# Performance work log

Measured on AMD Instinct MI355X. Metric: run time of the kernel, lower is better.

Reference implementation:

```python
import jax, jax.numpy as jnp
import numpy as np

K = 3          # kernel size
STRIDE = 1
PAD = 1
DIL = 1


def setup_inputs() -> dict:
    key = jax.random.key(0)
    k1, k2, k3 = jax.random.split(key, 3)
    N, Cin, H, W = 8, 128, 64, 64
    Cout = 128
    x = jax.random.normal(k1, (N, Cin, H, W), dtype=jnp.float32)
    # offset channels: 2 * deformable_groups * K*K = 18, interleaved (dy, dx) per tap
    offset = jax.random.normal(k2, (N, 2 * K * K, H, W), dtype=jnp.float32)
    weight = jax.random.normal(k3, (Cout, Cin, K, K), dtype=jnp.float32) / np.sqrt(Cin * K * K)
    return {"x": x, "offset": offset, "weight": weight}


def _deform_conv(x, offset, weight):
    N, Cin, H, W = x.shape
    Cout = weight.shape[0]
    KK = K * K
    Ho, Wo = offset.shape[2], offset.shape[3]

    off = offset.reshape(N, KK, 2, Ho, Wo)
    dy = off[:, :, 0]  # [N, KK, Ho, Wo]
    dx = off[:, :, 1]

    kh = jnp.repeat(jnp.arange(K), K).astype(x.dtype)   # [KK]
    kw = jnp.tile(jnp.arange(K), K).astype(x.dtype)     # [KK]
    base_i = (jnp.arange(Ho) * STRIDE - PAD).astype(x.dtype)  # [Ho]
    base_j = (jnp.arange(Wo) * STRIDE - PAD).astype(x.dtype)  # [Wo]

    # Sampling positions: [N, KK, Ho, Wo]
    py = base_i[None, None, :, None] + (kh * DIL)[None, :, None, None] + dy
    px = base_j[None, None, None, :] + (kw * DIL)[None, :, None, None] + dx

    y0 = jnp.floor(py)
    x0 = jnp.floor(px)
    wy1 = py - y0
    wx1 = px - x0
    wy0 = 1.0 - wy1
    wx0 = 1.0 - wx1
    y0i = y0.astype(jnp.int32)
    x0i = x0.astype(jnp.int32)
    y1i = y0i + 1
    x1i = x0i + 1

    x_flat = x.reshape(N, Cin, H * W)

    def gather(yi, xi):
        # zero-padding outside the image
        mask = ((yi >= 0) & (yi < H) & (xi >= 0) & (xi < W)).astype(x.dtype)
        idx = jnp.clip(yi, 0, H - 1) * W + jnp.clip(xi, 0, W - 1)  # [N,KK,Ho,Wo]
        v = jnp.take_along_axis(x_flat, idx.reshape(N, 1, -1), axis=2)  # [N,Cin,KK*Ho*Wo]
        v = v.reshape(N, Cin, KK, Ho, Wo)
        return v * mask[:, None]

    sampled = (gather(y0i, x0i) * (wy0 * wx0)[:, None]
               + gather(y0i, x1i) * (wy0 * wx1)[:, None]
               + gather(y1i, x0i) * (wy1 * wx0)[:, None]
               + gather(y1i, x1i) * (wy1 * wx1)[:, None])  # [N,Cin,KK,Ho,Wo]

    w = weight.reshape(Cout, Cin, KK)
    return jnp.einsum('nckij,ock->noij', sampled, w)


def reference(x, offset, weight):
    return _deform_conv(x, offset, weight)
```

## Files before the change

kernel.cpp:

```cpp
#include <hip/hip_runtime.h>


#define H  64
#define W  64
#define CIN 128
#define COUT 128
#define NB 8
#define KK 9
#define SROW (CIN + 8)

typedef short bf16x8 __attribute__((ext_vector_type(8)));
typedef float f32x4  __attribute__((ext_vector_type(4)));

__device__ __forceinline__ unsigned short f2bf(float f) {
    unsigned u = __builtin_bit_cast(unsigned, f);
    u += 0x7FFFu + ((u >> 16) & 1u);
    return (unsigned short)(u >> 16);
}
__device__ __forceinline__ unsigned cvt_pk_bf16(float lo, float hi) {
    unsigned r;
    asm("v_cvt_pk_bf16_f32 %0, %1, %2" : "=v"(r) : "v"(lo), "v"(hi));
    return r;
}
__device__ __forceinline__ float lo_f(unsigned u) { return __builtin_bit_cast(float, u << 16); }
__device__ __forceinline__ float hi_f(unsigned u) { return __builtin_bit_cast(float, u & 0xFFFF0000u); }

__global__ void prep_all(const float* __restrict__ x, const float* __restrict__ w,
                         unsigned short* __restrict__ xt, unsigned short* __restrict__ wt) {
    int b = blockIdx.x;
    int t = threadIdx.x;
    if (b >= NB * H) {
        int idx = (b - NB * H) * 256 + t;
        if (idx < KK * COUT * CIN) {
            int e  = idx & 7;
            int lq = (idx >> 3) & 3;
            int lm = (idx >> 5) & 15;
            int ct = (idx >> 9) & 3;
            int nt = (idx >> 11) & 1;
            int c4 = (idx >> 12) & 3;
            int kk = idx >> 14;
            int co = (c4 << 5) + (nt << 4) + lm;
            int ch = (ct << 5) + (lq << 3) + e;
            wt[idx] = f2bf(w[(co * CIN + ch) * KK + kk]);
        }
        return;
    }
    __shared__ float tile[CIN][W + 4];
    int n = b & 7, y = b >> 3;
    const float* src = x + ((size_t)n * CIN * H + y) * W;
    #pragma unroll
    for (int it = 0; it < 8; ++it) {
        int idx = it * 256 + t;
        int c  = idx >> 4;
        int x4 = (idx & 15) << 2;
        int xs = (x4 + ((c >> 5) << 4)) & 63;
        *(float4*)&tile[c][xs] = *(const float4*)(src + (size_t)c * H * W + x4);
    }
    __syncthreads();
    int xp = t >> 2;
    int cbch = (t & 3) << 5;
    int xr = (xp + ((cbch >> 5) << 4)) & 63;
    unsigned short* dst = xt + (((size_t)(n * H + y) * W + xp) * CIN + cbch);
    unsigned rr[16];
    #pragma unroll
    for (int i = 0; i < 16; ++i)
        rr[i] = cvt_pk_bf16(tile[cbch + 2 * i][xr], tile[cbch + 2 * i + 1][xr]);
    #pragma unroll
    for (int i = 0; i < 4; ++i)
        ((uint4*)dst)[i] = make_uint4(rr[4*i], rr[4*i+1], rr[4*i+2], rr[4*i+3]);
}

struct GatherCtx {
    const unsigned short *c00, *c01, *c10, *c11;
    float w00, w01, w10, w11;
};

__device__ __forceinline__ GatherCtx gather_setup(float dy, float dx, int ho, int wo, int kk,
                                                  const unsigned short* xbase) {
    GatherCtx g;
    float py = (float)(ho - 1 + kk / 3) + dy;
    float px = (float)(wo - 1 + kk % 3) + dx;
    float y0f = floorf(py), x0f = floorf(px);
    float wy1 = py - y0f, wx1 = px - x0f;
    float wy0 = 1.f - wy1, wx0 = 1.f - wx1;
    int y0 = (int)y0f, x0 = (int)x0f;
    int y1 = y0 + 1, x1 = x0 + 1;
    bool vy0 = (unsigned)y0 < (unsigned)H, vy1 = (unsigned)y1 < (unsigned)H;
    bool vx0 = (unsigned)x0 < (unsigned)W, vx1 = (unsigned)x1 < (unsigned)W;
    g.w00 = (vy0 && vx0) ? wy0 * wx0 : 0.f;
    g.w01 = (vy0 && vx1) ? wy0 * wx1 : 0.f;
    g.w10 = (vy1 && vx0) ? wy1 * wx0 : 0.f;
    g.w11 = (vy1 && vx1) ? wy1 * wx1 : 0.f;
    int yc0 = min(max(y0, 0), H - 1), yc1 = min(max(y1, 0), H - 1);
    int xc0 = min(max(x0, 0), W - 1), xc1 = min(max(x1, 0), W - 1);
    const unsigned short* r0 = xbase + (size_t)yc0 * W * CIN;
    const unsigned short* r1 = xbase + (size_t)yc1 * W * CIN;
    g.c00 = r0 + xc0 * CIN;  g.c01 = r0 + xc1 * CIN;
    g.c10 = r1 + xc0 * CIN;  g.c11 = r1 + xc1 * CIN;
    return g;
}

__global__ __launch_bounds__(512, 2) void sample_k(
        const float* __restrict__ offs, const unsigned short* __restrict__ xt,
        unsigned short* __restrict__ S) {
    int b = blockIdx.x;
    int n = b & 7;
    int r = b >> 3;
    int tap = r >> 6;
    int ho = r & 63;
    int t = threadIdx.x;
    int pos = t >> 3;
    int cb = (t & 7) << 4;

    const float* offp = offs + ((size_t)(n * 2 * KK + 2 * tap) * H + ho) * W + pos;
    float dy = offp[0];
    float dx = offp[(size_t)H * W];

    GatherCtx g = gather_setup(dy, dx, ho, pos, tap, xt + (size_t)n * H * W * CIN + cb);

    uint4 gv[8];
    #pragma unroll
    for (int j = 0; j < 2; ++j) {
        gv[4*j+0] = *(const uint4*)(g.c00 + 8*j);
        gv[4*j+1] = *(const uint4*)(g.c01 + 8*j);
        gv[4*j+2] = *(const uint4*)(g.c10 + 8*j);
        gv[4*j+3] = *(const uint4*)(g.c11 + 8*j);
    }
    unsigned rr[8];
    #pragma unroll
    for (int j = 0; j < 2; ++j) {
        const unsigned* a0 = (const unsigned*)&gv[4*j+0];
        const unsigned* a1 = (const unsigned*)&gv[4*j+1];
        const unsigned* a2 = (const unsigned*)&gv[4*j+2];
        const unsigned* a3 = (const unsigned*)&gv[4*j+3];
        #pragma unroll
        for (int i = 0; i < 4; ++i) {
            float v0 = g.w00*lo_f(a0[i]) + g.w01*lo_f(a1[i]) + g.w10*lo_f(a2[i]) + g.w11*lo_f(a3[i]);
            float v1 = g.w00*hi_f(a0[i]) + g.w01*hi_f(a1[i]) + g.w10*hi_f(a2[i]) + g.w11*hi_f(a3[i]);
            rr[4*j+i] = cvt_pk_bf16(v0, v1);
        }
    }
    size_t so = ((((size_t)(n * H + ho) * W + pos) * KK + tap) << 7) + cb;
    *(uint4*)(S + so)     = make_uint4(rr[0], rr[1], rr[2], rr[3]);
    *(uint4*)(S + so + 8) = make_uint4(rr[4], rr[5], rr[6], rr[7]);
}

__global__ __launch_bounds__(256, 2) void gemm_k(
        const unsigned short* __restrict__ S, const unsigned short* __restrict__ wt,
        float* __restrict__ out) {
    __shared__ __attribute__((aligned(16))) unsigned short samp[2][64][SROW];

    int b = blockIdx.x;
    int n = b & 7, ho = b >> 3;
    int t = threadIdx.x;
    int lane = t & 63, wv = t >> 6;
    int lm = lane & 15, lq = lane >> 4;
    int cobase = wv << 5;
    int slot = (lm << 2) + lq;

    f32x4 acc[4][2];
    #pragma unroll
    for (int mt = 0; mt < 4; ++mt)
        #pragma unroll
        for (int nt = 0; nt < 2; ++nt) acc[mt][nt] = f32x4{0.f, 0.f, 0.f, 0.f};

    int pos = t >> 2;
    int seg = t & 3;
    const unsigned short* srow = S + ((((size_t)(n * H + ho) * W + pos) * KK) << 7) + (seg << 5);
    const unsigned short* wvbase = wt + ((size_t)wv << 12) + (slot << 3);

    {
        uint4 st[4];
        #pragma unroll
        for (int i = 0; i < 4; ++i) st[i] = *(const uint4*)(srow + (i << 3));
        unsigned short* ld = &samp[0][pos][seg << 5];
        #pragma unroll
        for (int i = 0; i < 4; ++i) *(uint4*)(ld + (i << 3)) = st[i];
    }
    __syncthreads();

    for (int tap = 0; tap < KK; ++tap) {
        uint4 nx[4];
        if (tap < KK - 1) {
            const unsigned short* sr = srow + ((size_t)(tap + 1) << 7);
            #pragma unroll
            for (int i = 0; i < 4; ++i) nx[i] = *(const uint4*)(sr + (i << 3));
        }
        const unsigned short* wkb = wvbase + ((size_t)tap << 14);
        bf16x8 bW[2][4];
        #pragma unroll
        for (int nt = 0; nt < 2; ++nt)
            #pragma unroll
            for (int ct = 0; ct < 4; ++ct)
                bW[nt][ct] = *(const bf16x8*)(wkb + (((nt << 2) + ct) << 9));

        #pragma unroll
        for (int ct = 0; ct < 4; ++ct) {
            bf16x8 a[4];
            #pragma unroll
            for (int mt = 0; mt < 4; ++mt)
                a[mt] = *(const bf16x8*)&samp[tap & 1][lm + (mt << 4)][(ct << 5) + (lq << 3)];
            #pragma unroll
            for (int mt = 0; mt < 4; ++mt) {
                acc[mt][0] = __builtin_amdgcn_mfma_f32_16x16x32_bf16(a[mt], bW[0][ct], acc[mt][0], 0, 0, 0);
                acc[mt][1] = __builtin_amdgcn_mfma_f32_16x16x32_bf16(a[mt], bW[1][ct], acc[mt][1], 0, 0, 0);
            }
        }
        if (tap < KK - 1) {
            unsigned short* ld = &samp[(tap + 1) & 1][pos][seg << 5];
            #pragma unroll
            for (int i = 0; i < 4; ++i) *(uint4*)(ld + (i << 3)) = nx[i];
        }
        __syncthreads();
    }

    #pragma unroll
    for (int mt = 0; mt < 4; ++mt) {
        int wob = (mt << 4) + (lq << 2);
        #pragma unroll
        for (int nt = 0; nt < 2; ++nt) {
            int co = cobase + (nt << 4) + lm;
            *(f32x4*)(out + (((size_t)(n * COUT + co) * H + ho) * W + wob)) = acc[mt][nt];
        }
    }
}

extern "C" void kernel_launch(void* const* d_in, const int* in_sizes, int n_in,
                              void* d_out, int out_size, void* d_ws, size_t ws_size,
                              hipStream_t stream) {
    const float* x      = (const float*)d_in[0];
    const float* offset = (const float*)d_in[1];
    const float* weight = (const float*)d_in[2];
    float* out = (float*)d_out;

    unsigned short* xt = (unsigned short*)d_ws;
    unsigned short* wt = (unsigned short*)((char*)d_ws + 8388608);
    unsigned short* S  = (unsigned short*)((char*)d_ws + 8683520);

    int wblocks = (KK * COUT * CIN + 255) / 256;
    hipLaunchKernelGGL(prep_all, dim3(NB * H + wblocks), dim3(256), 0, stream,
                       x, weight, xt, wt);
    hipLaunchKernelGGL(sample_k, dim3(NB * KK * H), dim3(512), 0, stream,
                       offset, xt, S);
    hipLaunchKernelGGL(gemm_k, dim3(NB * H), dim3(256), 0, stream,
                       S, wt, out);
}
```

Before: 116.6 us.

## Fuse deformable sampling and GEMM into a single kernel per output row

Merges the separate bilinear-sampling kernel and the MFMA GEMM kernel into one launch. Each 512-thread block now samples all nine taps for its (n, ho) row, writes them to the global scratch buffer, then reads them back through double-buffered LDS for the GEMM. The GEMM work is spread over eight waves of 16 output channels each instead of four waves of 32. This removes one kernel launch and the inter-kernel gap, and the readback should mostly hit cache. In exchange, the gather runs serially over taps with far fewer blocks than before, which may expose memory latency and reduce parallelism.

```diff
diff --git a/kernel.cpp b/kernel.cpp
--- a/kernel.cpp
+++ b/kernel.cpp
@@ -100,53 +100,9 @@
     return g;
 }
 
-__global__ __launch_bounds__(512, 2) void sample_k(
+__global__ __launch_bounds__(512, 4) void fused_main(
         const float* __restrict__ offs, const unsigned short* __restrict__ xt,
-        unsigned short* __restrict__ S) {
-    int b = blockIdx.x;
-    int n = b & 7;
-    int r = b >> 3;
-    int tap = r >> 6;
-    int ho = r & 63;
-    int t = threadIdx.x;
-    int pos = t >> 3;
-    int cb = (t & 7) << 4;
-
-    const float* offp = offs + ((size_t)(n * 2 * KK + 2 * tap) * H + ho) * W + pos;
-    float dy = offp[0];
-    float dx = offp[(size_t)H * W];
-
-    GatherCtx g = gather_setup(dy, dx, ho, pos, tap, xt + (size_t)n * H * W * CIN + cb);
-
-    uint4 gv[8];
-    #pragma unroll
-    for (int j = 0; j < 2; ++j) {
-        gv[4*j+0] = *(const uint4*)(g.c00 + 8*j);
-        gv[4*j+1] = *(const uint4*)(g.c01 + 8*j);
-        gv[4*j+2] = *(const uint4*)(g.c10 + 8*j);
-        gv[4*j+3] = *(const uint4*)(g.c11 + 8*j);
-    }
-    unsigned rr[8];
-    #pragma unroll
-    for (int j = 0; j < 2; ++j) {
-        const unsigned* a0 = (const unsigned*)&gv[4*j+0];
-        const unsigned* a1 = (const unsigned*)&gv[4*j+1];
-        const unsigned* a2 = (const unsigned*)&gv[4*j+2];
-        const unsigned* a3 = (const unsigned*)&gv[4*j+3];
-        #pragma unroll
-        for (int i = 0; i < 4; ++i) {
-            float v0 = g.w00*lo_f(a0[i]) + g.w01*lo_f(a1[i]) + g.w10*lo_f(a2[i]) + g.w11*lo_f(a3[i]);
-            float v1 = g.w00*hi_f(a0[i]) + g.w01*hi_f(a1[i]) + g.w10*hi_f(a2[i]) + g.w11*hi_f(a3[i]);
-            rr[4*j+i] = cvt_pk_bf16(v0, v1);
-        }
-    }
-    size_t so = ((((size_t)(n * H + ho) * W + pos) * KK + tap) << 7) + cb;
-    *(uint4*)(S + so)     = make_uint4(rr[0], rr[1], rr[2], rr[3]);
-    *(uint4*)(S + so + 8) = make_uint4(rr[4], rr[5], rr[6], rr[7]);
-}
-
-__global__ __launch_bounds__(256, 2) void gemm_k(
-        const unsigned short* __restrict__ S, const unsigned short* __restrict__ wt,
+        const unsigned short* __restrict__ wt, unsigned short* __restrict__ S,
         float* __restrict__ out) {
     __shared__ __attribute__((aligned(16))) unsigned short samp[2][64][SROW];
 
@@ -155,44 +111,76 @@
     int t = threadIdx.x;
     int lane = t & 63, wv = t >> 6;
     int lm = lane & 15, lq = lane >> 4;
-    int cobase = wv << 5;
+
+    int pos = t >> 3;
+    int c16 = t & 7;
+    int cb  = c16 << 4;
+
+    const float* offp = offs + (size_t)n * 2 * KK * H * W + (size_t)ho * W + pos;
+    const unsigned short* xb = xt + (size_t)n * H * W * CIN + cb;
+    size_t srow = ((((size_t)(n * H + ho) * W + pos) * KK) << 7) + cb;
+
+    for (int tap = 0; tap < KK; ++tap) {
+        float dy = offp[(size_t)(2 * tap) * H * W];
+        float dx = offp[(size_t)(2 * tap + 1) * H * W];
+        GatherCtx g = gather_setup(dy, dx, ho, pos, tap, xb);
+        uint4 gv[8];
+        #pragma unroll
+        for (int j = 0; j < 2; ++j) {
+            gv[4*j+0] = *(const uint4*)(g.c00 + 8*j);
+            gv[4*j+1] = *(const uint4*)(g.c01 + 8*j);
+            gv[4*j+2] = *(const uint4*)(g.c10 + 8*j);
+            gv[4*j+3] = *(const uint4*)(g.c11 + 8*j);
+        }
+        unsigned rr[8];
+        #pragma unroll
+        for (int j = 0; j < 2; ++j) {
+            const unsigned* a0 = (const unsigned*)&gv[4*j+0];
+            const unsigned* a1 = (const unsigned*)&gv[4*j+1];
+            const unsigned* a2 = (const unsigned*)&gv[4*j+2];
+            const unsigned* a3 = (const unsigned*)&gv[4*j+3];
+            #pragma unroll
+            for (int i = 0; i < 4; ++i) {
+                float v0 = g.w00*lo_f(a0[i]) + g.w01*lo_f(a1[i]) + g.w10*lo_f(a2[i]) + g.w11*lo_f(a3[i]);
+                float v1 = g.w00*hi_f(a0[i]) + g.w01*hi_f(a1[i]) + g.w10*hi_f(a2[i]) + g.w11*hi_f(a3[i]);
+                rr[4*j+i] = cvt_pk_bf16(v0, v1);
+            }
+        }
+        unsigned short* sp = S + srow + ((size_t)tap << 7);
+        *(uint4*)(sp)     = make_uint4(rr[0], rr[1], rr[2], rr[3]);
+        *(uint4*)(sp + 8) = make_uint4(rr[4], rr[5], rr[6], rr[7]);
+    }
+    asm volatile("s_waitcnt vmcnt(0)" ::: "memory");
+
+    f32x4 acc[4];
+    #pragma unroll
+    for (int mt = 0; mt < 4; ++mt) acc[mt] = f32x4{0.f, 0.f, 0.f, 0.f};
+
     int slot = (lm << 2) + lq;
-
-    f32x4 acc[4][2];
-    #pragma unroll
-    for (int mt = 0; mt < 4; ++mt)
-        #pragma unroll
-        for (int nt = 0; nt < 2; ++nt) acc[mt][nt] = f32x4{0.f, 0.f, 0.f, 0.f};
-
-    int pos = t >> 2;
-    int seg = t & 3;
-    const unsigned short* srow = S + ((((size_t)(n * H + ho) * W + pos) * KK) << 7) + (seg << 5);
-    const unsigned short* wvbase = wt + ((size_t)wv << 12) + (slot << 3);
+    const unsigned short* wvbase = wt + ((size_t)wv << 11) + (slot << 3);
+    const unsigned short* sme = S + srow;
 
     {
-        uint4 st[4];
-        #pragma unroll
-        for (int i = 0; i < 4; ++i) st[i] = *(const uint4*)(srow + (i << 3));
-        unsigned short* ld = &samp[0][pos][seg << 5];
-        #pragma unroll
-        for (int i = 0; i < 4; ++i) *(uint4*)(ld + (i << 3)) = st[i];
+        uint4 s0 = *(const uint4*)(sme);
+        uint4 s1 = *(const uint4*)(sme + 8);
+        unsigned short* ld = &samp[0][pos][cb];
+        *(uint4*)(ld)     = s0;
+        *(uint4*)(ld + 8) = s1;
     }
     __syncthreads();
 
     for (int tap = 0; tap < KK; ++tap) {
-        uint4 nx[4];
+        uint4 nx0, nx1;
         if (tap < KK - 1) {
-            const unsigned short* sr = srow + ((size_t)(tap + 1) << 7);
-            #pragma unroll
-            for (int i = 0; i < 4; ++i) nx[i] = *(const uint4*)(sr + (i << 3));
-        }
-        const unsigned short* wkb = wvbase + ((size_t)tap << 14);
-        bf16x8 bW[2][4];
-        #pragma unroll
-        for (int nt = 0; nt < 2; ++nt)
-            #pragma unroll
-            for (int ct = 0; ct < 4; ++ct)
-                bW[nt][ct] = *(const bf16x8*)(wkb + (((nt << 2) + ct) << 9));
+            const unsigned short* sr = sme + ((size_t)(tap + 1) << 7);
+            nx0 = *(const uint4*)(sr);
+            nx1 = *(const uint4*)(sr + 8);
+        }
+        const unsigned short* wkb = wvbase + ((size_t)(tap << 3) << 11);
+        bf16x8 bW[4];
+        #pragma unroll
+        for (int ct = 0; ct < 4; ++ct)
+            bW[ct] = *(const bf16x8*)(wkb + (ct << 9));
 
         #pragma unroll
         for (int ct = 0; ct < 4; ++ct) {
@@ -201,27 +189,22 @@
             for (int mt = 0; mt < 4; ++mt)
                 a[mt] = *(const bf16x8*)&samp[tap & 1][lm + (mt << 4)][(ct << 5) + (lq << 3)];
             #pragma unroll
-            for (int mt = 0; mt < 4; ++mt) {
-                acc[mt][0] = __builtin_amdgcn_mfma_f32_16x16x32_bf16(a[mt], bW[0][ct], acc[mt][0], 0, 0, 0);
-                acc[mt][1] = __builtin_amdgcn_mfma_f32_16x16x32_bf16(a[mt], bW[1][ct], acc[mt][1], 0, 0, 0);
-            }
+            for (int mt = 0; mt < 4; ++mt)
+                acc[mt] = __builtin_amdgcn_mfma_f32_16x16x32_bf16(a[mt], bW[ct], acc[mt], 0, 0, 0);
         }
         if (tap < KK - 1) {
-            unsigned short* ld = &samp[(tap + 1) & 1][pos][seg << 5];
-            #pragma unroll
-            for (int i = 0; i < 4; ++i) *(uint4*)(ld + (i << 3)) = nx[i];
+            unsigned short* ld = &samp[(tap + 1) & 1][pos][cb];
+            *(uint4*)(ld)     = nx0;
+            *(uint4*)(ld + 8) = nx1;
         }
         __syncthreads();
     }
 
+    int co = (wv << 4) + lm;
     #pragma unroll
     for (int mt = 0; mt < 4; ++mt) {
         int wob = (mt << 4) + (lq << 2);
-        #pragma unroll
-        for (int nt = 0; nt < 2; ++nt) {
-            int co = cobase + (nt << 4) + lm;
-            *(f32x4*)(out + (((size_t)(n * COUT + co) * H + ho) * W + wob)) = acc[mt][nt];
-        }
+        *(f32x4*)(out + (((size_t)(n * COUT + co) * H + ho) * W + wob)) = acc[mt];
     }
 }
 
@@ -240,8 +223,6 @@
     int wblocks = (KK * COUT * CIN + 255) / 256;
     hipLaunchKernelGGL(prep_all, dim3(NB * H + wblocks), dim3(256), 0, stream,
                        x, weight, xt, wt);
-    hipLaunchKernelGGL(sample_k, dim3(NB * KK * H), dim3(512), 0, stream,
-                       offset, xt, S);
-    hipLaunchKernelGGL(gemm_k, dim3(NB * H), dim3(256), 0, stream,
-                       S, wt, out);
-}
+    hipLaunchKernelGGL(fused_main, dim3(NB * H), dim3(512), 0, stream,
+                       offset, xt, wt, S, out);
+}
```

New measurement: 109.3 us. -6.3%, faster.
